# Performance work log

Measured on AMD Instinct MI355X. Metric: run time of the kernel, lower is better.

Reference implementation:

```python
import jax, jax.numpy as jnp
import numpy as np

TAU = 2.0        # LIF membrane time constant
VTH = 1.0        # firing threshold
ALPHA = 4.0      # surrogate sigmoid sharpness
BN_EPS = 1e-5

@jax.custom_vjp
def heaviside_surrogate(x):
    # Forward: hard threshold. Backward: sigmoid surrogate gradient (alpha=4).
    return (x >= 0.0).astype(x.dtype)

def _hs_fwd(x):
    return heaviside_surrogate(x), x

def _hs_bwd(x, g):
    s = jax.nn.sigmoid(ALPHA * x)
    return (g * ALPHA * s * (1.0 - s),)

heaviside_surrogate.defvjp(_hs_fwd, _hs_bwd)


def setup_inputs() -> dict:
    key = jax.random.key(0)
    k1, k2 = jax.random.split(key)
    B, Cin, T, Cout = 64, 512, 1024, 256
    x = jax.random.normal(k1, (B, Cin, T), dtype=jnp.float32)
    W = jax.random.normal(k2, (Cout, Cin), dtype=jnp.float32) * (1.0 / np.sqrt(Cin))
    gamma = jnp.ones((Cout,), dtype=jnp.float32)
    beta = jnp.zeros((Cout,), dtype=jnp.float32)
    run_mean = jnp.zeros((Cout,), dtype=jnp.float32)
    run_var = jnp.ones((Cout,), dtype=jnp.float32)
    return {"x": x, "W": W, "gamma": gamma, "beta": beta,
            "run_mean": run_mean, "run_var": run_var}


def reference(x, W, gamma, beta, run_mean, run_var):
    # Dropout is identity in eval mode.
    # conv1d, kernel_size=1, no bias -> pointwise GEMM over channels: [B,Cin,T] -> [B,Cout,T]
    y = jnp.einsum('bct,oc->bot', x, W)
    # BatchNorm1d (inference, running stats), per-channel affine
    inv = jax.lax.rsqrt(run_var + BN_EPS)
    y = (y - run_mean[None, :, None]) * (inv * gamma)[None, :, None] + beta[None, :, None]
    # LIF recurrence over the time dim (last axis), hard reset to 0, detach_reset.
    yt = jnp.transpose(y, (2, 0, 1))  # [T, B, Cout]

    def step(v, x_t):
        v = v + (x_t - v) / TAU              # decay_input charge
        s = heaviside_surrogate(v - VTH)     # spike via surrogate threshold
        v = v * (1.0 - jax.lax.stop_gradient(s))  # hard reset (detached)
        return v, s

    v0 = jnp.zeros(yt.shape[1:], dtype=yt.dtype)
    _, spikes = jax.lax.scan(step, v0, yt)   # spikes: [T, B, Cout]
    # out.mean(dim=-1) == spike rate over time
    return spikes.mean(axis=0)               # [B, Cout]
```

## Files before the change

kernel.cpp:

```cpp
#include <hip/hip_runtime.h>
#include <math.h>

typedef _Float16 f16;
typedef __attribute__((ext_vector_type(8)))  _Float16 f16v8;
typedef __attribute__((ext_vector_type(16))) float    f32x16;
typedef __attribute__((ext_vector_type(4)))  float    f32x4;

namespace {
constexpr int kB = 64, kCin = 512, kT = 1024, kCout = 256;
constexpr size_t kYBytes     = (size_t)kB * kT * kCout * 4;
constexpr size_t kWfragBytes = (size_t)32 * 8 * 2 * 64 * 16;
constexpr size_t kSBytes     = kCout * 4;
constexpr size_t kWsNeed     = kYBytes + kWfragBytes + kSBytes;
}

__global__ void wsplit16_kernel(const float* __restrict__ W, f16* __restrict__ wfrag) {
    const int kc = blockIdx.x, osub = blockIdx.y, p = blockIdx.z;
    const int lane = threadIdx.x;
    const int o  = osub * 32 + (lane & 31);
    const int kb = kc * 16 + (lane >> 5) * 8;
    f16v8 frag;
#pragma unroll
    for (int j = 0; j < 8; ++j) {
        const float w = 32.0f * W[o * kCin + kb + j];
        const f16 h = (f16)w;
        const float r = w - (float)h;
        const f16 l = (f16)(r * 2048.0f);
        frag[j] = p ? l : h;
    }
    *reinterpret_cast<f16v8*>(wfrag + ((size_t)((kc * 8 + osub) * 2 + p) * 64 + lane) * 8) = frag;
}

__global__ void sprep_kernel(const float* __restrict__ gamma, const float* __restrict__ rvar,
                             float* __restrict__ sarr) {
    const int o = threadIdx.x;
    sarr[o] = (float)((double)gamma[o] / sqrt((double)rvar[o] + 1e-5));
}

__global__ __launch_bounds__(512, 2)
void gemm_f16_kernel(const float* __restrict__ x, const f16* __restrict__ wfrag,
                     const float* __restrict__ sarr, const float* __restrict__ rmean,
                     const float* __restrict__ beta, float* __restrict__ y) {
    __shared__ union {
        f16   B[2][2][64 * 24];
        float tb[8][32 * 36];
    } sh;

    const int tid  = threadIdx.x;
    const int lane = tid & 63;
    const int wave = tid >> 6;
    const int wo = wave >> 1, wt = wave & 1;
    const int n = lane & 31, q = lane >> 5;
    const int b   = blockIdx.y;
    const int tg0 = blockIdx.x * 64;
    const int o0  = wo * 64;
    const float* __restrict__ xb = x + ((size_t)b << 19);
    const f16v8* __restrict__ wf = reinterpret_cast<const f16v8*>(wfrag);

    const int st_t = lane;
    const int st_k = wave;
    const int wrow = st_t * 24 + 2 * (st_k ^ ((st_t >> 3 & 1) << 2));
    const int tloc = wt * 32 + n;
    const int rrow = tloc * 24 + 8 * (q ^ (tloc >> 3 & 1));

    f32x16 accA[2] = {};
    f32x16 accB[2] = {};
    f16v8  af[2][2][2];
    float  x0a, x1a;

    auto loadX = [&](int kc) {
        const float* px = xb + (size_t)(kc * 16 + 2 * st_k) * kT + tg0 + st_t;
        x0a = px[0];
        x1a = px[kT];
    };
    auto loadA = [&](int kc, f16v8 (&ad)[2][2]) {
#pragma unroll
        for (int i = 0; i < 2; ++i)
#pragma unroll
            for (int p = 0; p < 2; ++p)
                ad[i][p] = wf[(size_t)((kc * 8 + wo * 2 + i) * 2 + p) * 64 + lane];
    };
    auto stage = [&](int buf) {
        auto h2 = __builtin_amdgcn_cvt_pkrtz(x0a, x1a);
        const float r0 = x0a - (float)h2[0];
        const float r1 = x1a - (float)h2[1];
        auto l2 = __builtin_amdgcn_cvt_pkrtz(r0 * 2048.0f, r1 * 2048.0f);
        *reinterpret_cast<decltype(h2)*>(&sh.B[buf][0][wrow]) = h2;
        *reinterpret_cast<decltype(l2)*>(&sh.B[buf][1][wrow]) = l2;
    };
    auto domfma = [&](int buf, const f16v8 (&ad)[2][2]) {
        const f16v8 bh = *reinterpret_cast<const f16v8*>(&sh.B[buf][0][rrow]);
        const f16v8 bl = *reinterpret_cast<const f16v8*>(&sh.B[buf][1][rrow]);
#pragma unroll
        for (int i = 0; i < 2; ++i) {
            accA[i] = __builtin_amdgcn_mfma_f32_32x32x16_f16(ad[i][0], bh, accA[i], 0, 0, 0);
            accB[i] = __builtin_amdgcn_mfma_f32_32x32x16_f16(ad[i][0], bl, accB[i], 0, 0, 0);
            accB[i] = __builtin_amdgcn_mfma_f32_32x32x16_f16(ad[i][1], bh, accB[i], 0, 0, 0);
        }
    };

    loadX(0);
    loadA(0, af[0]);
    stage(0);
    loadX(1);
    __syncthreads();

#pragma unroll 2
    for (int kc = 0; kc < 32; ++kc) {
        const int cur = kc & 1, nxt = cur ^ 1;
        if (kc < 31) loadA(kc + 1, af[nxt]);
        if (kc < 31) stage(nxt);
        if (kc < 30) loadX(kc + 2);
        domfma(cur, af[cur]);
        __syncthreads();
    }

    float* tb = sh.tb[wave];
#pragma unroll
    for (int i = 0; i < 2; ++i) {
        const f32x16 v = accA[i] + accB[i] * 4.8828125e-4f;
        asm volatile("s_waitcnt lgkmcnt(0)" ::: "memory");
#pragma unroll
        for (int g = 0; g < 4; ++g) {
            f32x4 t4;
            t4.x = v[4 * g + 0]; t4.y = v[4 * g + 1];
            t4.z = v[4 * g + 2]; t4.w = v[4 * g + 3];
            *reinterpret_cast<f32x4*>(tb + n * 36 + g * 8 + q * 4) = t4;
        }
        asm volatile("s_waitcnt lgkmcnt(0)" ::: "memory");
#pragma unroll
        for (int r4 = 0; r4 < 4; ++r4) {
            const int fidx = lane + 64 * r4;
            const int tl = fidx >> 3, o4 = fidx & 7;
            const int og = o0 + i * 32 + o4 * 4;
            f32x4 val = *reinterpret_cast<const f32x4*>(tb + tl * 36 + o4 * 4);
            const f32x4 sv = *reinterpret_cast<const f32x4*>(sarr + og);
            const f32x4 mv = *reinterpret_cast<const f32x4*>(rmean + og);
            const f32x4 bv = *reinterpret_cast<const f32x4*>(beta + og);
            val = (val * 0.03125f - mv) * sv + bv;
            const size_t t = (size_t)tg0 + wt * 32 + tl;
            *reinterpret_cast<f32x4*>(y + ((((size_t)b << 10) + t) << 8) + og) = val;
        }
    }
}

__global__ __launch_bounds__(64)
void lif_kernel(const float* __restrict__ y, float* __restrict__ out) {
    const int b = blockIdx.x >> 2;
    const int o = ((blockIdx.x & 3) << 6) + threadIdx.x;
    const float* __restrict__ yb = y + ((size_t)b << 18);
    float v = 0.f;
    int cnt = 0;
    float b0[32], b1[32];
    auto loadb = [&](int i, float (&buf)[32]) {
#pragma unroll
        for (int j = 0; j < 32; ++j)
            buf[j] = yb[(size_t)(i * 32 + j) * 256 + o];
    };
    auto stepb = [&](const float (&buf)[32]) {
#pragma unroll
        for (int j = 0; j < 32; ++j) {
            v = v + (buf[j] - v) * 0.5f;
            if (v - 1.0f >= 0.0f) { ++cnt; v = 0.f; }
        }
    };
    loadb(0, b0);
    for (int bb = 0; bb < 16; ++bb) {
        loadb(2 * bb + 1, b1);
        stepb(b0);
        if (bb < 15) loadb(2 * bb + 2, b0);
        stepb(b1);
    }
    out[((size_t)b << 8) + o] = (float)cnt * (1.0f / 1024.0f);
}

namespace fb {
constexpr int kOTile = 32, kTTile = 128, kCc = 64;
constexpr int kNtt = kT / kTTile, kNcc = kCin / kCc, kYPad = 132;
}

__global__ void wt_transpose_kernel(const float* __restrict__ W, float* __restrict__ Wt) {
    int idx = blockIdx.x * 256 + threadIdx.x;
    int c = idx >> 8, o = idx & 255;
    Wt[idx] = W[o * kCin + c];
}

__global__ __launch_bounds__(256, 2)
void snn_fused_kernel(const float* __restrict__ x, const float* __restrict__ Wt,
                      const float* __restrict__ gamma, const float* __restrict__ beta,
                      const float* __restrict__ rmean, const float* __restrict__ rvar,
                      float* __restrict__ out) {
    using namespace fb;
    __shared__ float xs[kCc][kTTile];
    __shared__ float ws[kCc][kOTile];
    __shared__ float ytile[kOTile][kYPad];
    __shared__ float sarr[kOTile], barr[kOTile], marr[kOTile], vstate[kOTile];
    __shared__ int scnt[kOTile];
    const int tid = threadIdx.x, tx = tid & 31, ty = tid >> 5;
    const int b = blockIdx.y, o_blk = blockIdx.x * kOTile;
    if (tid < kOTile) {
        const int o = o_blk + tid;
        const double dinv = 1.0 / sqrt((double)rvar[o] + 1e-5);
        sarr[tid] = (float)(dinv * (double)gamma[o]);
        barr[tid] = beta[o]; marr[tid] = rmean[o];
        vstate[tid] = 0.0f; scnt[tid] = 0;
    }
    __syncthreads();
    const float* xb = x + (size_t)b * kCin * kT;
    for (int tt = 0; tt < kNtt; ++tt) {
        float acc[4][4];
#pragma unroll
        for (int i = 0; i < 4; ++i)
#pragma unroll
            for (int j = 0; j < 4; ++j) acc[i][j] = 0.0f;
        const int t0 = tt * kTTile;
        for (int cc = 0; cc < kNcc; ++cc) {
#pragma unroll
            for (int k = 0; k < 8; ++k) {
                const int f = tid + 256 * k;
                const int c = f >> 5, tq = f & 31;
                *reinterpret_cast<float4*>(&xs[c][tq * 4]) = *reinterpret_cast<const float4*>(
                    xb + (size_t)(cc * kCc + c) * kT + t0 + tq * 4);
            }
#pragma unroll
            for (int k = 0; k < 2; ++k) {
                const int f = tid + 256 * k;
                const int c = f >> 3, oq = f & 7;
                *reinterpret_cast<float4*>(&ws[c][oq * 4]) = *reinterpret_cast<const float4*>(
                    Wt + (size_t)(cc * kCc + c) * kCout + o_blk + oq * 4);
            }
            __syncthreads();
#pragma unroll 8
            for (int c = 0; c < kCc; ++c) {
                const float4 xv = *reinterpret_cast<const float4*>(&xs[c][tx * 4]);
                const float4 wv = *reinterpret_cast<const float4*>(&ws[c][ty * 4]);
                const float xf[4] = {xv.x, xv.y, xv.z, xv.w};
                const float wf4[4] = {wv.x, wv.y, wv.z, wv.w};
#pragma unroll
                for (int i = 0; i < 4; ++i)
#pragma unroll
                    for (int j = 0; j < 4; ++j) acc[i][j] += wf4[i] * xf[j];
            }
            __syncthreads();
        }
#pragma unroll
        for (int i = 0; i < 4; ++i) {
            const int o = ty * 4 + i;
            const float s = sarr[o], bb2 = barr[o], m = marr[o];
#pragma unroll
            for (int j = 0; j < 4; ++j) ytile[o][tx * 4 + j] = (acc[i][j] - m) * s + bb2;
        }
        __syncthreads();
        if (tid < kOTile) {
            float vv = vstate[tid];
            int cnt = 0;
#pragma unroll 4
            for (int t = 0; t < kTTile; ++t) {
                const float yv = ytile[tid][t];
                vv = vv + (yv - vv) * 0.5f;
                if (vv - 1.0f >= 0.0f) { cnt++; vv = 0.0f; }
            }
            vstate[tid] = vv; scnt[tid] += cnt;
        }
        __syncthreads();
    }
    if (tid < kOTile) out[b * kCout + o_blk + tid] = (float)scnt[tid] * (1.0f / 1024.0f);
}

extern "C" void kernel_launch(void* const* d_in, const int* in_sizes, int n_in,
                              void* d_out, int out_size, void* d_ws, size_t ws_size,
                              hipStream_t stream) {
    const float* x     = (const float*)d_in[0];
    const float* W     = (const float*)d_in[1];
    const float* gamma = (const float*)d_in[2];
    const float* beta  = (const float*)d_in[3];
    const float* rmean = (const float*)d_in[4];
    const float* rvar  = (const float*)d_in[5];
    float* out = (float*)d_out;

    if (ws_size >= kWsNeed) {
        float* y     = (float*)d_ws;
        f16*   wfrag = (f16*)((char*)d_ws + kYBytes);
        float* sarr  = (float*)((char*)d_ws + kYBytes + kWfragBytes);
        sprep_kernel<<<1, 256, 0, stream>>>(gamma, rvar, sarr);
        wsplit16_kernel<<<dim3(32, 8, 2), 64, 0, stream>>>(W, wfrag);
        gemm_f16_kernel<<<dim3(16, 64), 512, 0, stream>>>(x, wfrag, sarr, rmean, beta, y);
        lif_kernel<<<256, 64, 0, stream>>>(y, out);
    } else {
        float* Wt = (float*)d_ws;
        wt_transpose_kernel<<<(kCin * kCout) / 256, 256, 0, stream>>>(W, Wt);
        snn_fused_kernel<<<dim3(kCout / fb::kOTile, kB), 256, 0, stream>>>(
            x, Wt, gamma, beta, rmean, rvar, out);
    }
}
```

Measured before the change: 263.9 us.

## Halve GEMM block threads so each wave covers full time tile; fold sprep into wsplit

The GEMM block drops from 8 waves to 4. Each wave now owns 64 output channels across both 32-step time subtiles, so every W fragment loaded into registers is reused across two B tiles, and each thread stages 4 input rows instead of 2. The shared-memory B layout is repacked into a single interleaved hi/lo buffer with a new swizzle. The separate BN-scale kernel is merged into the W-split kernel to save one launch. The cost is twice the accumulator registers per wave and fewer waves per block to hide latency.

```diff
diff --git a/kernel.cpp b/kernel.cpp
--- a/kernel.cpp
+++ b/kernel.cpp
@@ -3,6 +3,7 @@
 
 typedef _Float16 f16;
 typedef __attribute__((ext_vector_type(8)))  _Float16 f16v8;
+typedef __attribute__((ext_vector_type(4)))  __fp16   h16v4;
 typedef __attribute__((ext_vector_type(16))) float    f32x16;
 typedef __attribute__((ext_vector_type(4)))  float    f32x4;
 
@@ -14,7 +15,9 @@
 constexpr size_t kWsNeed     = kYBytes + kWfragBytes + kSBytes;
 }
 
-__global__ void wsplit16_kernel(const float* __restrict__ W, f16* __restrict__ wfrag) {
+__global__ void wsplit16_kernel(const float* __restrict__ W, const float* __restrict__ gamma,
+                                const float* __restrict__ rvar,
+                                f16* __restrict__ wfrag, float* __restrict__ sarr) {
     const int kc = blockIdx.x, osub = blockIdx.y, p = blockIdx.z;
     const int lane = threadIdx.x;
     const int o  = osub * 32 + (lane & 31);
@@ -29,119 +32,131 @@
         frag[j] = p ? l : h;
     }
     *reinterpret_cast<f16v8*>(wfrag + ((size_t)((kc * 8 + osub) * 2 + p) * 64 + lane) * 8) = frag;
-}
-
-__global__ void sprep_kernel(const float* __restrict__ gamma, const float* __restrict__ rvar,
-                             float* __restrict__ sarr) {
-    const int o = threadIdx.x;
-    sarr[o] = (float)((double)gamma[o] / sqrt((double)rvar[o] + 1e-5));
-}
-
-__global__ __launch_bounds__(512, 2)
+    if (kc == 0 && osub == 0 && p == 0) {
+#pragma unroll
+        for (int j = 0; j < 4; ++j) {
+            const int oo = j * 64 + lane;
+            sarr[oo] = (float)((double)gamma[oo] / sqrt((double)rvar[oo] + 1e-5));
+        }
+    }
+}
+
+__global__ __launch_bounds__(256, 2)
 void gemm_f16_kernel(const float* __restrict__ x, const f16* __restrict__ wfrag,
                      const float* __restrict__ sarr, const float* __restrict__ rmean,
                      const float* __restrict__ beta, float* __restrict__ y) {
     __shared__ union {
-        f16   B[2][2][64 * 24];
-        float tb[8][32 * 36];
+        unsigned int Bd[2][64 * 20];
+        float        tb[4][32 * 36];
     } sh;
 
     const int tid  = threadIdx.x;
     const int lane = tid & 63;
     const int wave = tid >> 6;
-    const int wo = wave >> 1, wt = wave & 1;
     const int n = lane & 31, q = lane >> 5;
     const int b   = blockIdx.y;
     const int tg0 = blockIdx.x * 64;
-    const int o0  = wo * 64;
     const float* __restrict__ xb = x + ((size_t)b << 19);
     const f16v8* __restrict__ wf = reinterpret_cast<const f16v8*>(wfrag);
 
-    const int st_t = lane;
-    const int st_k = wave;
-    const int wrow = st_t * 24 + 2 * (st_k ^ ((st_t >> 3 & 1) << 2));
-    const int tloc = wt * 32 + n;
-    const int rrow = tloc * 24 + 8 * (q ^ (tloc >> 3 & 1));
-
-    f32x16 accA[2] = {};
-    f32x16 accB[2] = {};
+    const int st_t = tid & 63;
+    const int kpp  = wave;
+    const int st_sw = (st_t >> 3) & 3;
+    const int wr_base = 20 * st_t + 2 * (kpp & 1);
+    const int s0 = ((0 + (kpp >> 1)) ^ st_sw) * 4;
+    const int s1 = ((2 + (kpp >> 1)) ^ st_sw) * 4;
+
+    f32x16 accA[2][2] = {};
+    f32x16 accB[2][2] = {};
     f16v8  af[2][2][2];
-    float  x0a, x1a;
-
-    auto loadX = [&](int kc) {
-        const float* px = xb + (size_t)(kc * 16 + 2 * st_k) * kT + tg0 + st_t;
-        x0a = px[0];
-        x1a = px[kT];
+    float  xr[2][4];
+
+    auto loadX = [&](int kc, float (&xd)[4]) {
+        const float* px = xb + (size_t)(kc * 16 + 4 * kpp) * kT + tg0 + st_t;
+#pragma unroll
+        for (int r = 0; r < 4; ++r) xd[r] = px[(size_t)r * kT];
     };
     auto loadA = [&](int kc, f16v8 (&ad)[2][2]) {
 #pragma unroll
         for (int i = 0; i < 2; ++i)
 #pragma unroll
             for (int p = 0; p < 2; ++p)
-                ad[i][p] = wf[(size_t)((kc * 8 + wo * 2 + i) * 2 + p) * 64 + lane];
-    };
-    auto stage = [&](int buf) {
-        auto h2 = __builtin_amdgcn_cvt_pkrtz(x0a, x1a);
-        const float r0 = x0a - (float)h2[0];
-        const float r1 = x1a - (float)h2[1];
-        auto l2 = __builtin_amdgcn_cvt_pkrtz(r0 * 2048.0f, r1 * 2048.0f);
-        *reinterpret_cast<decltype(h2)*>(&sh.B[buf][0][wrow]) = h2;
-        *reinterpret_cast<decltype(l2)*>(&sh.B[buf][1][wrow]) = l2;
+                ad[i][p] = wf[(size_t)((kc * 8 + wave * 2 + i) * 2 + p) * 64 + lane];
+    };
+    auto stage = [&](int buf, const float (&xd)[4]) {
+        auto h01 = __builtin_amdgcn_cvt_pkrtz(xd[0], xd[1]);
+        auto h23 = __builtin_amdgcn_cvt_pkrtz(xd[2], xd[3]);
+        auto l01 = __builtin_amdgcn_cvt_pkrtz((xd[0] - (float)h01[0]) * 2048.0f,
+                                              (xd[1] - (float)h01[1]) * 2048.0f);
+        auto l23 = __builtin_amdgcn_cvt_pkrtz((xd[2] - (float)h23[0]) * 2048.0f,
+                                              (xd[3] - (float)h23[1]) * 2048.0f);
+        h16v4 hv, lv;
+        hv[0] = h01[0]; hv[1] = h01[1]; hv[2] = h23[0]; hv[3] = h23[1];
+        lv[0] = l01[0]; lv[1] = l01[1]; lv[2] = l23[0]; lv[3] = l23[1];
+        *reinterpret_cast<h16v4*>(&sh.Bd[buf][wr_base + s0]) = hv;
+        *reinterpret_cast<h16v4*>(&sh.Bd[buf][wr_base + s1]) = lv;
     };
     auto domfma = [&](int buf, const f16v8 (&ad)[2][2]) {
-        const f16v8 bh = *reinterpret_cast<const f16v8*>(&sh.B[buf][0][rrow]);
-        const f16v8 bl = *reinterpret_cast<const f16v8*>(&sh.B[buf][1][rrow]);
-#pragma unroll
-        for (int i = 0; i < 2; ++i) {
-            accA[i] = __builtin_amdgcn_mfma_f32_32x32x16_f16(ad[i][0], bh, accA[i], 0, 0, 0);
-            accB[i] = __builtin_amdgcn_mfma_f32_32x32x16_f16(ad[i][0], bl, accB[i], 0, 0, 0);
-            accB[i] = __builtin_amdgcn_mfma_f32_32x32x16_f16(ad[i][1], bh, accB[i], 0, 0, 0);
-        }
-    };
-
-    loadX(0);
+#pragma unroll
+        for (int s = 0; s < 2; ++s) {
+            const int t = s * 32 + n;
+            const int sw = (t >> 3) & 3;
+            const f16v8 bh = *reinterpret_cast<const f16v8*>(&sh.Bd[buf][20 * t + 4 * ((0 + q) ^ sw)]);
+            const f16v8 bl = *reinterpret_cast<const f16v8*>(&sh.Bd[buf][20 * t + 4 * ((2 + q) ^ sw)]);
+#pragma unroll
+            for (int i = 0; i < 2; ++i) {
+                accA[i][s] = __builtin_amdgcn_mfma_f32_32x32x16_f16(ad[i][0], bh, accA[i][s], 0, 0, 0);
+                accB[i][s] = __builtin_amdgcn_mfma_f32_32x32x16_f16(ad[i][0], bl, accB[i][s], 0, 0, 0);
+                accB[i][s] = __builtin_amdgcn_mfma_f32_32x32x16_f16(ad[i][1], bh, accB[i][s], 0, 0, 0);
+            }
+        }
+    };
+
+    loadX(0, xr[0]);
     loadA(0, af[0]);
-    stage(0);
-    loadX(1);
+    stage(0, xr[0]);
+    loadX(1, xr[1]);
     __syncthreads();
 
 #pragma unroll 2
     for (int kc = 0; kc < 32; ++kc) {
         const int cur = kc & 1, nxt = cur ^ 1;
         if (kc < 31) loadA(kc + 1, af[nxt]);
-        if (kc < 31) stage(nxt);
-        if (kc < 30) loadX(kc + 2);
+        if (kc < 31) stage(nxt, xr[nxt]);
+        if (kc < 30) loadX(kc + 2, xr[cur]);
         domfma(cur, af[cur]);
         __syncthreads();
     }
 
     float* tb = sh.tb[wave];
 #pragma unroll
-    for (int i = 0; i < 2; ++i) {
-        const f32x16 v = accA[i] + accB[i] * 4.8828125e-4f;
-        asm volatile("s_waitcnt lgkmcnt(0)" ::: "memory");
-#pragma unroll
-        for (int g = 0; g < 4; ++g) {
-            f32x4 t4;
-            t4.x = v[4 * g + 0]; t4.y = v[4 * g + 1];
-            t4.z = v[4 * g + 2]; t4.w = v[4 * g + 3];
-            *reinterpret_cast<f32x4*>(tb + n * 36 + g * 8 + q * 4) = t4;
-        }
-        asm volatile("s_waitcnt lgkmcnt(0)" ::: "memory");
-#pragma unroll
-        for (int r4 = 0; r4 < 4; ++r4) {
-            const int fidx = lane + 64 * r4;
-            const int tl = fidx >> 3, o4 = fidx & 7;
-            const int og = o0 + i * 32 + o4 * 4;
-            f32x4 val = *reinterpret_cast<const f32x4*>(tb + tl * 36 + o4 * 4);
-            const f32x4 sv = *reinterpret_cast<const f32x4*>(sarr + og);
-            const f32x4 mv = *reinterpret_cast<const f32x4*>(rmean + og);
-            const f32x4 bv = *reinterpret_cast<const f32x4*>(beta + og);
-            val = (val * 0.03125f - mv) * sv + bv;
-            const size_t t = (size_t)tg0 + wt * 32 + tl;
-            *reinterpret_cast<f32x4*>(y + ((((size_t)b << 10) + t) << 8) + og) = val;
-        }
-    }
+    for (int i = 0; i < 2; ++i)
+#pragma unroll
+        for (int s = 0; s < 2; ++s) {
+            const f32x16 v = accA[i][s] + accB[i][s] * 4.8828125e-4f;
+            asm volatile("s_waitcnt lgkmcnt(0)" ::: "memory");
+#pragma unroll
+            for (int g = 0; g < 4; ++g) {
+                f32x4 t4;
+                t4.x = v[4 * g + 0]; t4.y = v[4 * g + 1];
+                t4.z = v[4 * g + 2]; t4.w = v[4 * g + 3];
+                *reinterpret_cast<f32x4*>(tb + n * 36 + g * 8 + q * 4) = t4;
+            }
+            asm volatile("s_waitcnt lgkmcnt(0)" ::: "memory");
+#pragma unroll
+            for (int r4 = 0; r4 < 4; ++r4) {
+                const int fidx = lane + 64 * r4;
+                const int tl = fidx >> 3, o4 = fidx & 7;
+                const int og = wave * 64 + i * 32 + o4 * 4;
+                f32x4 val = *reinterpret_cast<const f32x4*>(tb + tl * 36 + o4 * 4);
+                const f32x4 sv = *reinterpret_cast<const f32x4*>(sarr + og);
+                const f32x4 mv = *reinterpret_cast<const f32x4*>(rmean + og);
+                const f32x4 bv = *reinterpret_cast<const f32x4*>(beta + og);
+                val = (val * 0.03125f - mv) * sv + bv;
+                const size_t t = (size_t)tg0 + s * 32 + tl;
+                *reinterpret_cast<f32x4*>(y + ((((size_t)b << 10) + t) << 8) + og) = val;
+            }
+        }
 }
 
 __global__ __launch_bounds__(64)
@@ -282,9 +297,8 @@
         float* y     = (float*)d_ws;
         f16*   wfrag = (f16*)((char*)d_ws + kYBytes);
         float* sarr  = (float*)((char*)d_ws + kYBytes + kWfragBytes);
-        sprep_kernel<<<1, 256, 0, stream>>>(gamma, rvar, sarr);
-        wsplit16_kernel<<<dim3(32, 8, 2), 64, 0, stream>>>(W, wfrag);
-        gemm_f16_kernel<<<dim3(16, 64), 512, 0, stream>>>(x, wfrag, sarr, rmean, beta, y);
+        wsplit16_kernel<<<dim3(32, 8, 2), 64, 0, stream>>>(W, gamma, rvar, wfrag, sarr);
+        gemm_f16_kernel<<<dim3(16, 64), 256, 0, stream>>>(x, wfrag, sarr, rmean, beta, y);
         lif_kernel<<<256, 64, 0, stream>>>(y, out);
     } else {
         float* Wt = (float*)d_ws;
```

After: 256.2 us. 2.9% less time.
